# Optimization experiments

Hardware: AMD Instinct MI355X
Metric: run time of the kernel (lower is better)

Reference implementation:

```python
import jax, jax.numpy as jnp
import numpy as np

TEMPERATURE = 0.1
NORM_EPS = 1e-12   # F.normalize default eps
LOSS_EPS = 1e-6

def _l2norm_c(x):
    # L2-normalize along channel dim (axis=1), matching F.normalize(dim=1)
    n = jnp.sqrt(jnp.sum(x * x, axis=1, keepdims=True))
    return x / jnp.maximum(n, NORM_EPS)

def setup_inputs() -> dict:
    key = jax.random.key(0)
    k1, k2, k3 = jax.random.split(key, 3)
    N, C, H, W = 8, 64, 64, 64
    rgb_map = jax.random.normal(k1, (N, C, H, W), dtype=jnp.float32)
    ir_map = jax.random.normal(k2, (N, C, H, W), dtype=jnp.float32)
    targets = jax.random.randint(k3, (N,), 0, 2)  # unused by the forward math
    return {"rgb_map": rgb_map, "ir_map": ir_map, "targets": targets}

def reference(rgb_map, ir_map, targets):
    N, C, H, W = rgb_map.shape
    rgb = _l2norm_c(rgb_map).reshape(N, C, H * W)   # [N, C, P]
    ir = _l2norm_c(ir_map).reshape(N, C, H * W)     # [N, C, P]
    # [N, P, P] similarity, then temperature exp
    logit = jnp.exp(jnp.einsum('ncp,ncq->npq', rgb, ir) / TEMPERATURE)
    pos = jnp.trace(logit, axis1=1, axis2=2)        # diagonal (positive) sum per sample
    tot = jnp.sum(logit, axis=(-1, -2))             # full row/col sum per sample
    loss = -jnp.log(pos / (tot + LOSS_EPS)).mean()
    return loss
```

## Files before the change

### kernel.cpp

```cpp
#include <hip/hip_runtime.h>

#define N_ 8
#define C_ 64
#define P_ 4096

typedef float f32x4 __attribute__((ext_vector_type(4)));
typedef short bf16x8 __attribute__((ext_vector_type(8)));

__device__ __forceinline__ unsigned short f2bf(float f) {
  unsigned int u = __builtin_bit_cast(unsigned int, f);
  u = (u + 0x7fffu + ((u >> 16) & 1u)) >> 16;
  return (unsigned short)u;
}

__global__ void __launch_bounds__(256) norm_transpose(
    const float* __restrict__ rgb, const float* __restrict__ ir,
    unsigned short* __restrict__ rgbnT, unsigned short* __restrict__ irnT) {
  const int idx = blockIdx.x * 256 + threadIdx.x;
  const int n = idx >> 12;
  const int p = idx & (P_ - 1);
  const float* src = (blockIdx.y == 0) ? rgb : ir;
  unsigned short* dst = (blockIdx.y == 0) ? rgbnT : irnT;
  const float SC = 14.4269504088896340736f;
  const float* col = src + (size_t)n * C_ * P_ + p;
  float v[C_];
  float ss = 0.f;
#pragma unroll
  for (int c = 0; c < C_; ++c) {
    v[c] = col[(size_t)c * P_];
    ss += v[c] * v[c];
  }
  float inv = 1.0f / fmaxf(sqrtf(ss), 1e-12f);
  if (blockIdx.y == 0) inv *= SC;
  const int gx = (blockIdx.y == 0) ? 0 : (p & 7);
  unsigned short* o = dst + ((size_t)n * P_ + p) * C_;
#pragma unroll
  for (int g = 0; g < 8; ++g) {
    bf16x8 pack;
#pragma unroll
    for (int j = 0; j < 8; ++j) pack[j] = (short)f2bf(v[g * 8 + j] * inv);
    *reinterpret_cast<bf16x8*>(o + (g ^ gx) * 8) = pack;
  }
}

__device__ __forceinline__ void stage_tile(const unsigned short* src,
                                           unsigned short* dst, int tid,
                                           int wid) {
#pragma unroll
  for (int r = 0; r < 2; ++r) {
    __builtin_amdgcn_global_load_lds(
        (const __attribute__((address_space(1))) void*)(src +
                                                        (size_t)(r * 256 + tid) * 8),
        (__attribute__((address_space(3))) void*)(dst + (r * 256 + wid * 64) * 8),
        16, 0, 0);
  }
}

__global__ void __launch_bounds__(256) gemm_exp_reduce(
    const unsigned short* __restrict__ aT, const unsigned short* __restrict__ bT,
    float* __restrict__ partials) {
  const int lin = blockIdx.x;
  const int n = lin & 7;
  const int local = lin >> 3;
  const int pc = local & 15;
  const int qc = local >> 4;
  const int tid = threadIdx.x;
  const int lane = tid & 63;
  const int wid = tid >> 6;
  const int pbase = pc * 256 + wid * 64;
  const int q0 = qc * 512;
  const unsigned short* A = aT + (size_t)n * P_ * C_;
  const unsigned short* B = bT + (size_t)n * P_ * C_;
  const int r16 = lane & 15;
  const int kofs = (lane >> 4) * 8;

  __shared__ __align__(16) unsigned short bs0[64 * 64];
  __shared__ __align__(16) unsigned short bs1[64 * 64];
  __shared__ __align__(16) unsigned short bs2[64 * 64];
  __shared__ __align__(16) unsigned short bs3[64 * 64];

  bf16x8 af[2][4];
#pragma unroll
  for (int ks = 0; ks < 2; ++ks)
#pragma unroll
    for (int mi = 0; mi < 4; ++mi)
      af[ks][mi] = *reinterpret_cast<const bf16x8*>(
          A + (size_t)(pbase + mi * 16 + r16) * C_ + ks * 32 + kofs);

  stage_tile(B + (size_t)(q0 + 0 * 64) * C_, bs0, tid, wid);
  stage_tile(B + (size_t)(q0 + 1 * 64) * C_, bs1, tid, wid);
  stage_tile(B + (size_t)(q0 + 2 * 64) * C_, bs2, tid, wid);

  unsigned short *pcur = bs0, *pnx1 = bs1, *pnx2 = bs2, *pnx3 = bs3;

  const f32x4 zc = (f32x4)(0.f);
  float t0 = 0.f, t1 = 0.f, t2 = 0.f, t3 = 0.f, pos = 0.f;
  const int col = lane & 15;
  const int rowb = (lane >> 4) * 4;

#pragma unroll 1
  for (int t = 0; t < 8; ++t) {
    asm volatile("s_waitcnt vmcnt(4)" ::: "memory");
    __builtin_amdgcn_sched_barrier(0);
    __builtin_amdgcn_s_barrier();

    int s = t + 3;
    if (s >= 8) s -= 8;
    stage_tile(B + (size_t)(q0 + s * 64) * C_, pnx3, tid, wid);

    const unsigned short* bp = pcur;
    bf16x8 bf_[2][4];
#pragma unroll
    for (int ks = 0; ks < 2; ++ks)
#pragma unroll
      for (int ni = 0; ni < 4; ++ni) {
        const int row = ni * 16 + r16;
        const int seg = ks * 4 + (lane >> 4);
        bf_[ks][ni] = *reinterpret_cast<const bf16x8*>(
            bp + row * 64 + ((seg ^ (lane & 7)) * 8));
      }

    f32x4 acc[4][4];
    __builtin_amdgcn_s_setprio(1);
#pragma unroll
    for (int mi = 0; mi < 4; ++mi)
#pragma unroll
      for (int ni = 0; ni < 4; ++ni)
        acc[mi][ni] = __builtin_amdgcn_mfma_f32_16x16x32_bf16(
            af[0][mi], bf_[0][ni], zc, 0, 0, 0);
#pragma unroll
    for (int mi = 0; mi < 4; ++mi)
#pragma unroll
      for (int ni = 0; ni < 4; ++ni)
        acc[mi][ni] = __builtin_amdgcn_mfma_f32_16x16x32_bf16(
            af[1][mi], bf_[1][ni], acc[mi][ni], 0, 0, 0);
    __builtin_amdgcn_s_setprio(0);

#pragma unroll
    for (int mi = 0; mi < 4; ++mi)
#pragma unroll
      for (int ni = 0; ni < 4; ++ni) {
        const f32x4 v = acc[mi][ni];
        t0 += __builtin_amdgcn_exp2f(v[0]);
        t1 += __builtin_amdgcn_exp2f(v[1]);
        t2 += __builtin_amdgcn_exp2f(v[2]);
        t3 += __builtin_amdgcn_exp2f(v[3]);
      }
    const int qb = q0 + t * 64;
    if (pbase == qb) {
#pragma unroll
      for (int mi = 0; mi < 4; ++mi)
#pragma unroll
        for (int r = 0; r < 4; ++r)
          if (rowb + r == col) pos += __builtin_amdgcn_exp2f(acc[mi][mi][r]);
    }

    unsigned short* tmp = pcur;
    pcur = pnx1;
    pnx1 = pnx2;
    pnx2 = pnx3;
    pnx3 = tmp;
  }

  float tot = (t0 + t1) + (t2 + t3);
#pragma unroll
  for (int off = 32; off > 0; off >>= 1) {
    tot += __shfl_down(tot, off);
    pos += __shfl_down(pos, off);
  }
  __shared__ float sb[8];
  if (lane == 0) { sb[wid * 2] = pos; sb[wid * 2 + 1] = tot; }
  __syncthreads();
  if (tid == 0) {
    const float pp = sb[0] + sb[2] + sb[4] + sb[6];
    const float tt = sb[1] + sb[3] + sb[5] + sb[7];
    const int bid = n * 128 + pc * 8 + qc;
    partials[bid * 2] = pp;
    partials[bid * 2 + 1] = tt;
  }
}

__global__ void __launch_bounds__(1024) finalize(
    const float* __restrict__ partials, float* __restrict__ out) {
  const int tid = threadIdx.x;
  const int lane = tid & 63, wid = tid >> 6;
  __shared__ float sp[16], st[16], sl[8];
  const int n = tid >> 7;
  const int i = tid & 127;
  float p = partials[(n * 128 + i) * 2];
  float t = partials[(n * 128 + i) * 2 + 1];
#pragma unroll
  for (int off = 32; off > 0; off >>= 1) {
    p += __shfl_down(p, off);
    t += __shfl_down(t, off);
  }
  if (lane == 0) { sp[wid] = p; st[wid] = t; }
  __syncthreads();
  if (tid < 8) {
    const float pp = sp[2 * tid] + sp[2 * tid + 1];
    const float tt = st[2 * tid] + st[2 * tid + 1];
    sl[tid] = -logf(pp / (tt + 1e-6f));
  }
  __syncthreads();
  if (tid == 0) {
    float loss = 0.f;
#pragma unroll
    for (int k = 0; k < 8; ++k) loss += sl[k];
    out[0] = loss * (1.0f / N_);
  }
}

extern "C" void kernel_launch(void* const* d_in, const int* in_sizes, int n_in,
                              void* d_out, int out_size, void* d_ws, size_t ws_size,
                              hipStream_t stream) {
  const float* rgb = (const float*)d_in[0];
  const float* ir = (const float*)d_in[1];
  float* out = (float*)d_out;

  unsigned short* rgbnT = (unsigned short*)d_ws;
  unsigned short* irnT = rgbnT + (size_t)N_ * P_ * C_;
  float* partials = (float*)(irnT + (size_t)N_ * P_ * C_);

  dim3 g1(N_ * P_ / 256, 2);
  norm_transpose<<<g1, 256, 0, stream>>>(rgb, ir, rgbnT, irnT);

  gemm_exp_reduce<<<1024, 256, 0, stream>>>(rgbnT, irnT, partials);

  finalize<<<1, 1024, 0, stream>>>(partials, out);
}
```

Before: 40.87 us.

## Fuse finalize into GEMM kernel via last-block atomic counter; widen exp accumulators

Removes the separate finalize launch by having each GEMM block increment a global atomic counter; the last block to finish reads all partials and computes the loss. A hipMemsetAsync resets the counter each call. The exp-sum accumulation is also split across 16 independent accumulators to shorten the dependency chain. This trades one kernel launch for a memset node plus threadfence/atomic overhead in every block.

```diff
diff --git a/kernel.cpp b/kernel.cpp
--- a/kernel.cpp
+++ b/kernel.cpp
@@ -58,7 +58,8 @@
 
 __global__ void __launch_bounds__(256) gemm_exp_reduce(
     const unsigned short* __restrict__ aT, const unsigned short* __restrict__ bT,
-    float* __restrict__ partials) {
+    float* __restrict__ partials, unsigned* __restrict__ counter,
+    float* __restrict__ out) {
   const int lin = blockIdx.x;
   const int n = lin & 7;
   const int local = lin >> 3;
@@ -94,7 +95,10 @@
   unsigned short *pcur = bs0, *pnx1 = bs1, *pnx2 = bs2, *pnx3 = bs3;
 
   const f32x4 zc = (f32x4)(0.f);
-  float t0 = 0.f, t1 = 0.f, t2 = 0.f, t3 = 0.f, pos = 0.f;
+  float ch[16];
+#pragma unroll
+  for (int k = 0; k < 16; ++k) ch[k] = 0.f;
+  float pos = 0.f;
   const int col = lane & 15;
   const int rowb = (lane >> 4) * 4;
 
@@ -140,11 +144,12 @@
     for (int mi = 0; mi < 4; ++mi)
 #pragma unroll
       for (int ni = 0; ni < 4; ++ni) {
+        const int base = ((mi * 4 + ni) & 3) * 4;
         const f32x4 v = acc[mi][ni];
-        t0 += __builtin_amdgcn_exp2f(v[0]);
-        t1 += __builtin_amdgcn_exp2f(v[1]);
-        t2 += __builtin_amdgcn_exp2f(v[2]);
-        t3 += __builtin_amdgcn_exp2f(v[3]);
+        ch[base + 0] += __builtin_amdgcn_exp2f(v[0]);
+        ch[base + 1] += __builtin_amdgcn_exp2f(v[1]);
+        ch[base + 2] += __builtin_amdgcn_exp2f(v[2]);
+        ch[base + 3] += __builtin_amdgcn_exp2f(v[3]);
       }
     const int qb = q0 + t * 64;
     if (pbase == qb) {
@@ -162,7 +167,10 @@
     pnx3 = tmp;
   }
 
-  float tot = (t0 + t1) + (t2 + t3);
+  float tot = ((ch[0] + ch[1]) + (ch[2] + ch[3])) +
+              ((ch[4] + ch[5]) + (ch[6] + ch[7])) +
+              (((ch[8] + ch[9]) + (ch[10] + ch[11])) +
+               ((ch[12] + ch[13]) + (ch[14] + ch[15])));
 #pragma unroll
   for (int off = 32; off > 0; off >>= 1) {
     tot += __shfl_down(tot, off);
@@ -177,36 +185,39 @@
     const int bid = n * 128 + pc * 8 + qc;
     partials[bid * 2] = pp;
     partials[bid * 2 + 1] = tt;
-  }
-}
-
-__global__ void __launch_bounds__(1024) finalize(
-    const float* __restrict__ partials, float* __restrict__ out) {
-  const int tid = threadIdx.x;
-  const int lane = tid & 63, wid = tid >> 6;
-  __shared__ float sp[16], st[16], sl[8];
-  const int n = tid >> 7;
-  const int i = tid & 127;
-  float p = partials[(n * 128 + i) * 2];
-  float t = partials[(n * 128 + i) * 2 + 1];
-#pragma unroll
-  for (int off = 32; off > 0; off >>= 1) {
-    p += __shfl_down(p, off);
-    t += __shfl_down(t, off);
-  }
-  if (lane == 0) { sp[wid] = p; st[wid] = t; }
+    __threadfence();
+  }
   __syncthreads();
-  if (tid < 8) {
-    const float pp = sp[2 * tid] + sp[2 * tid + 1];
-    const float tt = st[2 * tid] + st[2 * tid + 1];
-    sl[tid] = -logf(pp / (tt + 1e-6f));
-  }
+
+  __shared__ unsigned rank_s;
+  if (tid == 0) rank_s = atomicAdd(counter, 1u);
   __syncthreads();
-  if (tid == 0) {
-    float loss = 0.f;
-#pragma unroll
-    for (int k = 0; k < 8; ++k) loss += sl[k];
-    out[0] = loss * (1.0f / N_);
+  if (rank_s == 1023u) {
+    __threadfence();
+    __shared__ float rp[4], rt[4], rl;
+    if (tid == 0) rl = 0.f;
+    __syncthreads();
+    for (int nn = 0; nn < N_; ++nn) {
+      float p = 0.f, t2 = 0.f;
+      if (tid < 128) {
+        p = partials[(nn * 128 + tid) * 2];
+        t2 = partials[(nn * 128 + tid) * 2 + 1];
+      }
+#pragma unroll
+      for (int off = 32; off > 0; off >>= 1) {
+        p += __shfl_down(p, off);
+        t2 += __shfl_down(t2, off);
+      }
+      if (lane == 0) { rp[wid] = p; rt[wid] = t2; }
+      __syncthreads();
+      if (tid == 0) {
+        const float pp = (rp[0] + rp[1]) + (rp[2] + rp[3]);
+        const float tt = (rt[0] + rt[1]) + (rt[2] + rt[3]);
+        rl += -logf(pp / (tt + 1e-6f));
+      }
+      __syncthreads();
+    }
+    if (tid == 0) out[0] = rl * (1.0f / N_);
   }
 }
 
@@ -220,11 +231,13 @@
   unsigned short* rgbnT = (unsigned short*)d_ws;
   unsigned short* irnT = rgbnT + (size_t)N_ * P_ * C_;
   float* partials = (float*)(irnT + (size_t)N_ * P_ * C_);
+  unsigned* counter = (unsigned*)(partials + 2048);
+
+  hipMemsetAsync(counter, 0, sizeof(unsigned), stream);
 
   dim3 g1(N_ * P_ / 256, 2);
   norm_transpose<<<g1, 256, 0, stream>>>(rgb, ir, rgbnT, irnT);
 
-  gemm_exp_reduce<<<1024, 256, 0, stream>>>(rgbnT, irnT, partials);
-
-  finalize<<<1, 1024, 0, stream>>>(partials, out);
-}
+  gemm_exp_reduce<<<1024, 256, 0, stream>>>(rgbnT, irnT, partials, counter,
+                                            out);
+}
```

After: 63.46 us. 55.3% more time.
